# Performance work log

Measured on AMD Instinct MI355X. Metric: run time of the kernel, lower is better.

The kernel has to match this reference:

```python
import jax, jax.numpy as jnp
import numpy as np

C = 64
CR = C // 8  # reduced channels for Q/K


def _conv1x1(x, W, b):
    # 1x1 conv == per-pixel linear over channels: x [b,c,h,w], W [o,c], b [o]
    return jnp.einsum('bchw,oc->bohw', x, W) + b[None, :, None, None]


def setup_inputs() -> dict:
    key = jax.random.key(0)
    ks = jax.random.split(key, 12)
    b, c, h, w = 8, C, 48, 48
    s = 1.0 / np.sqrt(c)
    inp = {
        'x1': jax.random.normal(ks[0], (b, c, h, w), jnp.float32),
        'x2': jax.random.normal(ks[1], (b, c, h, w), jnp.float32),
        'Wqk1': jax.random.normal(ks[2], (2 * CR, c), jnp.float32) * s,
        'bqk1': jnp.zeros((2 * CR,), jnp.float32),
        'Wqk2': jax.random.normal(ks[3], (2 * CR, c), jnp.float32) * s,
        'bqk2': jnp.zeros((2 * CR,), jnp.float32),
        'Wv1': jax.random.normal(ks[4], (c, c), jnp.float32) * s,
        'bv1': jnp.zeros((c,), jnp.float32),
        'Wv2': jax.random.normal(ks[5], (c, c), jnp.float32) * s,
        'bv2': jnp.zeros((c,), jnp.float32),
        'gamma': jnp.zeros((1,), jnp.float32) + 0.1,  # nonzero so output depends on attn
        'beta': jnp.zeros((1,), jnp.float32) + 0.1,
    }
    return inp


def reference(x1, x2, Wqk1, bqk1, Wqk2, bqk2, Wv1, bv1, Wv2, bv2, gamma, beta):
    b, c, h, w = x1.shape
    n = h * w
    qk1 = _conv1x1(x1, Wqk1, bqk1)
    qk2 = _conv1x1(x2, Wqk2, bqk2)
    q1, k1 = qk1[:, :CR], qk1[:, CR:]
    q2, k2 = qk2[:, :CR], qk2[:, CR:]
    # flatten spatial: [b, cr, n]
    q1 = q1.reshape(b, CR, n); k1 = k1.reshape(b, CR, n)
    q2 = q2.reshape(b, CR, n); k2 = k2.reshape(b, CR, n)
    v1 = _conv1x1(x1, Wv1, bv1).reshape(b, c, n)
    v2 = _conv1x1(x2, Wv2, bv2).reshape(b, c, n)
    # attn[b,i,j] = softmax_j( q[:, :, i] . k[:, :, j] )
    attn1 = jax.nn.softmax(jnp.einsum('bci,bcj->bij', q1, k1), axis=-1)
    attn2 = jax.nn.softmax(jnp.einsum('bci,bcj->bij', q2, k2), axis=-1)
    # out[:, :, j] = sum_i v[:, :, i] * attn[:, i, j]
    o1 = jnp.einsum('bci,bij->bcj', v1, attn2).reshape(b, c, h, w) * gamma + x1
    o2 = jnp.einsum('bci,bij->bcj', v2, attn1).reshape(b, c, h, w) * beta + x2
    return (o1, o2)
```

## Files before the change

kernel.cpp:

```cpp
#include <hip/hip_runtime.h>
#include <hip/hip_bf16.h>

#define NB   8
#define CCH  64
#define CR8  8
#define NPX  2304
#define BCN  (NB*CCH*NPX)
#define LOG2E 1.4426950408889634f

typedef short  short8   __attribute__((ext_vector_type(8)));
typedef unsigned short ushort8t __attribute__((ext_vector_type(8)));
typedef float  float4t  __attribute__((ext_vector_type(4)));
typedef float  float16t __attribute__((ext_vector_type(16)));

static __device__ __forceinline__ float fexp2(float x) {
    return __builtin_amdgcn_exp2f(x);
}
static __device__ __forceinline__ unsigned short bf16r(float f) {
    return (unsigned short)((__float_as_uint(f) + 0x8000u) >> 16);
}
static __device__ __forceinline__ unsigned int pack_bf16(float lo, float hi) {
    const unsigned int ul = __float_as_uint(lo) + 0x8000u;
    const unsigned int uh = __float_as_uint(hi) + 0x8000u;
    return __builtin_amdgcn_perm(uh, ul, 0x07060302u);
}
static __device__ __forceinline__ short8 pack8(const float* f) {
    union { unsigned int u[4]; short8 s; } r;
    #pragma unroll
    for (int j = 0; j < 4; j++) r.u[j] = pack_bf16(f[2*j], f[2*j+1]);
    return r.s;
}

static __device__ __forceinline__ void build_bfrag(const float16t sc, short8* bf) {
    unsigned int d[4][2];
    #pragma unroll
    for (int q = 0; q < 4; q++) {
        #pragma unroll
        for (int m = 0; m < 2; m++)
            d[q][m] = pack_bf16(fexp2(sc[4*q + 2*m]), fexp2(sc[4*q + 2*m + 1]));
    }
    #pragma unroll
    for (int kp = 0; kp < 2; kp++) {
        union { unsigned int u[4]; short8 s; } r;
        #pragma unroll
        for (int m = 0; m < 2; m++) {
            unsigned int x = d[2*kp][m];
            unsigned int y = d[2*kp + 1][m];
            asm("v_permlane32_swap_b32 %0, %1" : "+v"(x), "+v"(y));
            r.u[m]     = x;
            r.u[2 + m] = y;
        }
        bf[kp] = r.s;
    }
}

#define WS_QB1 0
#define WS_KB1 (WS_QB1 + 147456)
#define WS_QB2 (WS_KB1 + 147456)
#define WS_KB2 (WS_QB2 + 147456)
#define WS_V1  (WS_KB2 + 147456)
#define WS_V2  (WS_V1 + BCN/2)

__global__ __launch_bounds__(256) void proj_kernel(
    const float* __restrict__ x1, const float* __restrict__ x2,
    const float* __restrict__ Wqk1, const float* __restrict__ bqk1,
    const float* __restrict__ Wqk2, const float* __restrict__ bqk2,
    const float* __restrict__ Wv1,  const float* __restrict__ bv1,
    const float* __restrict__ Wv2,  const float* __restrict__ bv2,
    float* __restrict__ ws, float* __restrict__ out)
{
    const int t    = threadIdx.x;
    const int lane = t & 63;
    const int w    = t >> 6;
    const int n16  = lane & 15;
    const int c4   = lane >> 4;
    const int nt   = w & 1;
    const int mh   = w >> 1;
    const int b    = blockIdx.y;
    const int px   = blockIdx.x * 32 + nt * 16 + n16;

    const float* xsb[2];
    xsb[0] = x1 + ((size_t)b * CCH) * NPX + px;
    xsb[1] = x2 + ((size_t)b * CCH) * NPX + px;

    float xr[2][16];
    short8 bfrag[2][2];
    #pragma unroll
    for (int st = 0; st < 2; st++) {
        #pragma unroll
        for (int ch = 0; ch < 2; ch++) {
            #pragma unroll
            for (int j = 0; j < 8; j++)
                xr[st][ch * 8 + j] = xsb[st][(ch * 32 + c4 * 8 + j) * NPX];
            bfrag[st][ch] = pack8(&xr[st][ch * 8]);
        }
    }

    if (mh == 0) {
        #pragma unroll
        for (int st = 0; st < 2; st++) {
            float* outs = out + (st ? (size_t)BCN : 0);
            #pragma unroll
            for (int e = 0; e < 16; e++) {
                const int ch = (e >> 3) * 32 + c4 * 8 + (e & 7);
                outs[((size_t)b * CCH + ch) * NPX + px] = xr[st][e];
            }
        }
    }

    float4t acc[5];
    #pragma unroll
    for (int mt = 0; mt < 5; mt++) { acc[mt][0]=0.f; acc[mt][1]=0.f; acc[mt][2]=0.f; acc[mt][3]=0.f; }

    #pragma unroll
    for (int mt = 0; mt < 5; mt++) {
        const int mi  = mh * 5 + mt;
        const int isqk = (mi < 2);
        const int st  = isqk ? (mi & 1) : (mi >= 6);
        const float* Wb;
        int rowbase;
        if (isqk) { Wb = (mi == 0) ? Wqk1 : Wqk2; rowbase = 0; }
        else      { Wb = (mi >= 6) ? Wv2 : Wv1; rowbase = (mi - (mi >= 6 ? 6 : 2)) * 16; }
        const float* wrow = Wb + (size_t)(rowbase + n16) * 64 + c4 * 8;

        const short8 bf0 = st ? bfrag[1][0] : bfrag[0][0];
        const short8 bf1 = st ? bfrag[1][1] : bfrag[0][1];

        #pragma unroll
        for (int ch = 0; ch < 2; ch++) {
            float fa[8];
            const float4 a0 = *(const float4*)(wrow + ch * 32);
            const float4 a1 = *(const float4*)(wrow + ch * 32 + 4);
            fa[0] = a0.x; fa[1] = a0.y; fa[2] = a0.z; fa[3] = a0.w;
            fa[4] = a1.x; fa[5] = a1.y; fa[6] = a1.z; fa[7] = a1.w;
            acc[mt] = __builtin_amdgcn_mfma_f32_16x16x32_bf16(
                pack8(fa), ch ? bf1 : bf0, acc[mt], 0, 0, 0);
        }
    }

    #pragma unroll
    for (int mt = 0; mt < 5; mt++) {
        const int mi = mh * 5 + mt;
        if (mi < 2) {
            const int st = mi & 1;
            const float* bqk = st ? bqk2 : bqk1;
            unsigned short* qb = (unsigned short*)(ws + (st ? WS_QB2 : WS_QB1));
            unsigned short* kb = (unsigned short*)(ws + (st ? WS_KB2 : WS_KB1));
            const size_t rbase = (size_t)(b * NPX + px) * 16;
            #pragma unroll
            for (int r = 0; r < 4; r++) {
                const int oc = c4 * 4 + r;
                const float val = acc[mt][r] + bqk[oc];
                if (oc < 8)
                    qb[rbase + oc] = bf16r(val * LOG2E);
                else
                    kb[rbase + (oc - 8)] = bf16r(val);
            }
            ushort8t zq, zk;
            #pragma unroll
            for (int e = 0; e < 8; e++) { zq[e] = 0; zk[e] = 0; }
            zk[0] = 0x3F80; zk[1] = 0x3F80;
            if (c4 == 0) *(ushort8t*)(qb + rbase + 8) = zq;
            if (c4 == 2) *(ushort8t*)(kb + rbase + 8) = zk;
        } else {
            const int st = (mi >= 6);
            const int vt_ = mi - (st ? 6 : 2);
            const float* bv = st ? bv2 : bv1;
            unsigned short* v = (unsigned short*)(ws + (st ? WS_V2 : WS_V1));
            #pragma unroll
            for (int r = 0; r < 4; r++) {
                const int oc = vt_ * 16 + c4 * 4 + r;
                const float val = acc[mt][r] + bv[oc];
                v[((size_t)b * CCH + oc) * NPX + px] = bf16r(val);
            }
        }
    }
}

__global__ __launch_bounds__(256) void stats_kernel(float* __restrict__ ws)
{
    const int t  = threadIdx.x;
    const int w  = t >> 6;
    const int n  = t & 31;
    const int h  = (t & 63) >> 5;
    const int ig = blockIdx.x;
    const int ab = blockIdx.y;
    const int b  = ab & 7;
    const int a  = ab >> 3;

    unsigned short* qbw = (unsigned short*)(ws + (a ? WS_QB2 : WS_QB1));
    const unsigned short* qb = qbw;
    const unsigned short* kb = (const unsigned short*)(ws + (a ? WS_KB2 : WS_KB1));

    __shared__ float red[4][32];

    const short8 qf = *(const short8*)(qb + (size_t)(b * NPX + ig * 32 + n) * 16 + h * 8);

    const unsigned short* kp = kb + (size_t)(b * NPX + w * 576 + n) * 16 + h * 8;
    short8 kf = *(const short8*)kp;

    float ssum = 0.f;
    for (int jc = 0; jc < 18; jc++) {
        kp += 512;
        short8 kn = kf;
        if (jc + 1 < 18) kn = *(const short8*)kp;
        float16t acc = {};
        acc = __builtin_amdgcn_mfma_f32_32x32x16_bf16(kf, qf, acc, 0, 0, 0);
        float s0 = 0.f, s1 = 0.f, s2 = 0.f, s3 = 0.f;
        #pragma unroll
        for (int r = 0; r < 4; r++) {
            s0 += fexp2(acc[4 * r + 0]);
            s1 += fexp2(acc[4 * r + 1]);
            s2 += fexp2(acc[4 * r + 2]);
            s3 += fexp2(acc[4 * r + 3]);
        }
        ssum += (s0 + s1) + (s2 + s3);
        kf = kn;
    }
    ssum += __shfl_xor(ssum, 32);
    if (h == 0) red[w][n] = ssum;
    __syncthreads();

    if (t < 32) {
        const float d = (red[0][t] + red[1][t]) + (red[2][t] + red[3][t]);
        const float m = -__log2f(d);
        const unsigned short mhi = bf16r(m);
        __hip_bfloat16 hb; *(unsigned short*)&hb = mhi;
        const unsigned short mlo = bf16r(m - __bfloat162float(hb));
        const size_t rbase = (size_t)(b * NPX + ig * 32 + t) * 16;
        qbw[rbase + 8] = mhi;
        qbw[rbase + 9] = mlo;
    }
}

__global__ __launch_bounds__(256) void out_kernel(
    const float* __restrict__ gamma, const float* __restrict__ beta,
    const float* __restrict__ ws, float* __restrict__ out)
{
    const int t  = threadIdx.x;
    const int jt = blockIdx.x;
    const int b  = blockIdx.y;
    const int z  = blockIdx.z;
    const int o  = z >> 1;
    const int g  = z & 1;

    const int a = o ? 0 : 1;
    const unsigned short* qb = (const unsigned short*)(ws + (a ? WS_QB2 : WS_QB1));
    const unsigned short* kb = (const unsigned short*)(ws + (a ? WS_KB2 : WS_KB1));
    const unsigned short* v  = (const unsigned short*)(ws + (o ? WS_V2 : WS_V1));
    const float  scale = o ? beta[0] : gamma[0];

    __shared__ unsigned short vt[2][64][72];

    const int lane = t & 63;
    const int w    = t >> 6;
    const int n    = lane & 31;
    const int h    = lane >> 5;
    const int jh   = w & 1;
    const int ih   = w >> 1;

    const int j0 = jt * 64 + jh * 32;

    const short8 kfrag = *(const short8*)(kb + (size_t)(b * NPX + j0 + n) * 16 + h * 8);

    const int c0 = t >> 3, s80 = (t & 7) * 8;
    const int c1 = (t + 256) >> 3, s81 = ((t + 256) & 7) * 8;

    const int ibase = g * 1152;
    const unsigned short* vp0 = v + ((size_t)b * CCH + c0) * NPX + ibase + s80;
    const unsigned short* vp1 = v + ((size_t)b * CCH + c1) * NPX + ibase + s81;
    const unsigned short* qp  = qb + (size_t)(b * NPX + ibase + ih * 32 + n) * 16 + h * 8;

    {
        const float4 va = *(const float4*)vp0;
        const float4 vb = *(const float4*)vp1;
        *(float4*)&vt[0][c0][s80] = va;
        *(float4*)&vt[0][c1][s81] = vb;
    }
    short8 qf = *(const short8*)qp;

    float16t oacc0 = {}, oacc1 = {};
    int cur = 0;

    for (int it = 0; it < 18; it++) {
        vp0 += 64; vp1 += 64; qp += 64 * 16;
        float4 vn0, vn1;
        short8 qn = qf;
        if (it + 1 < 18) {
            vn0 = *(const float4*)vp0;
            vn1 = *(const float4*)vp1;
            qn  = *(const short8*)qp;
        }

        __syncthreads();

        float16t sc = {};
        sc = __builtin_amdgcn_mfma_f32_32x32x16_bf16(qf, kfrag, sc, 0, 0, 0);

        short8 bf[2];
        build_bfrag(sc, bf);

        {
            const short8 a0 = *(const short8*)&vt[cur][n][ih * 32 + 0 * 16 + h * 8];
            const short8 a1 = *(const short8*)&vt[cur][32 + n][ih * 32 + 0 * 16 + h * 8];
            oacc0 = __builtin_amdgcn_mfma_f32_32x32x16_bf16(a0, bf[0], oacc0, 0, 0, 0);
            oacc1 = __builtin_amdgcn_mfma_f32_32x32x16_bf16(a1, bf[0], oacc1, 0, 0, 0);
            const short8 a2 = *(const short8*)&vt[cur][n][ih * 32 + 1 * 16 + h * 8];
            const short8 a3 = *(const short8*)&vt[cur][32 + n][ih * 32 + 1 * 16 + h * 8];
            oacc0 = __builtin_amdgcn_mfma_f32_32x32x16_bf16(a2, bf[1], oacc0, 0, 0, 0);
            oacc1 = __builtin_amdgcn_mfma_f32_32x32x16_bf16(a3, bf[1], oacc1, 0, 0, 0);
        }

        if (it + 1 < 18) {
            *(float4*)&vt[cur ^ 1][c0][s80] = vn0;
            *(float4*)&vt[cur ^ 1][c1][s81] = vn1;
        }

        qf = qn;
        cur ^= 1;
    }

    __syncthreads();
    float* comb = (float*)&vt[0][0][0];
    float* cb = comb + (size_t)jh * 2304 + (size_t)lane * 36;
    if (ih == 1) {
        *(float4*)(cb +  0) = *((const float4*)&oacc0 + 0);
        *(float4*)(cb +  4) = *((const float4*)&oacc0 + 1);
        *(float4*)(cb +  8) = *((const float4*)&oacc0 + 2);
        *(float4*)(cb + 12) = *((const float4*)&oacc0 + 3);
        *(float4*)(cb + 16) = *((const float4*)&oacc1 + 0);
        *(float4*)(cb + 20) = *((const float4*)&oacc1 + 1);
        *(float4*)(cb + 24) = *((const float4*)&oacc1 + 2);
        *(float4*)(cb + 28) = *((const float4*)&oacc1 + 3);
    }
    __syncthreads();
    if (ih == 0) {
        #pragma unroll
        for (int q = 0; q < 4; q++) {
            const float4 p0 = *(const float4*)(cb + q * 4);
            const float4 p1 = *(const float4*)(cb + 16 + q * 4);
            oacc0[4*q+0] += p0.x; oacc0[4*q+1] += p0.y; oacc0[4*q+2] += p0.z; oacc0[4*q+3] += p0.w;
            oacc1[4*q+0] += p1.x; oacc1[4*q+1] += p1.y; oacc1[4*q+2] += p1.z; oacc1[4*q+3] += p1.w;
        }
        float* outp = out + (o ? BCN : 0) + (b * CCH) * NPX + j0 + n;
        #pragma unroll
        for (int r = 0; r < 16; r++) {
            const int row = (r & 3) + 8 * (r >> 2) + 4 * h;
            atomicAdd(outp + row * NPX, oacc0[r] * scale);
            atomicAdd(outp + (32 + row) * NPX, oacc1[r] * scale);
        }
    }
}

extern "C" void kernel_launch(void* const* d_in, const int* in_sizes, int n_in,
                              void* d_out, int out_size, void* d_ws, size_t ws_size,
                              hipStream_t stream)
{
    const float* x1   = (const float*)d_in[0];
    const float* x2   = (const float*)d_in[1];
    const float* Wqk1 = (const float*)d_in[2];
    const float* bqk1 = (const float*)d_in[3];
    const float* Wqk2 = (const float*)d_in[4];
    const float* bqk2 = (const float*)d_in[5];
    const float* Wv1  = (const float*)d_in[6];
    const float* bv1  = (const float*)d_in[7];
    const float* Wv2  = (const float*)d_in[8];
    const float* bv2  = (const float*)d_in[9];
    const float* gamma = (const float*)d_in[10];
    const float* beta  = (const float*)d_in[11];
    float* out = (float*)d_out;
    float* ws  = (float*)d_ws;

    proj_kernel<<<dim3(72, 8), 256, 0, stream>>>(
        x1, x2, Wqk1, bqk1, Wqk2, bqk2, Wv1, bv1, Wv2, bv2, ws, out);
    stats_kernel<<<dim3(72, 16), 256, 0, stream>>>(ws);
    out_kernel<<<dim3(36, 8, 4), 256, 0, stream>>>(gamma, beta, ws, out);
}
```

Measured before the change: 138.3 us.

## Split output kernel across channel halves instead of key-range halves, drop atomics

```diff
diff --git a/kernel.cpp b/kernel.cpp
--- a/kernel.cpp
+++ b/kernel.cpp
@@ -250,7 +250,7 @@
     const unsigned short* v  = (const unsigned short*)(ws + (o ? WS_V2 : WS_V1));
     const float  scale = o ? beta[0] : gamma[0];
 
-    __shared__ unsigned short vt[2][64][72];
+    __shared__ unsigned short vt[2][32][72];
 
     const int lane = t & 63;
     const int w    = t >> 6;
@@ -259,36 +259,28 @@
     const int jh   = w & 1;
     const int ih   = w >> 1;
 
-    const int j0 = jt * 64 + jh * 32;
+    const int j0    = jt * 64 + jh * 32;
+    const int cbase = g * 32;
 
     const short8 kfrag = *(const short8*)(kb + (size_t)(b * NPX + j0 + n) * 16 + h * 8);
 
     const int c0 = t >> 3, s80 = (t & 7) * 8;
-    const int c1 = (t + 256) >> 3, s81 = ((t + 256) & 7) * 8;
-
-    const int ibase = g * 1152;
-    const unsigned short* vp0 = v + ((size_t)b * CCH + c0) * NPX + ibase + s80;
-    const unsigned short* vp1 = v + ((size_t)b * CCH + c1) * NPX + ibase + s81;
-    const unsigned short* qp  = qb + (size_t)(b * NPX + ibase + ih * 32 + n) * 16 + h * 8;
-
-    {
-        const float4 va = *(const float4*)vp0;
-        const float4 vb = *(const float4*)vp1;
-        *(float4*)&vt[0][c0][s80] = va;
-        *(float4*)&vt[0][c1][s81] = vb;
-    }
+
+    const unsigned short* vp0 = v + ((size_t)b * CCH + cbase + c0) * NPX + s80;
+    const unsigned short* qp  = qb + (size_t)(b * NPX + ih * 32 + n) * 16 + h * 8;
+
+    *(float4*)&vt[0][c0][s80] = *(const float4*)vp0;
     short8 qf = *(const short8*)qp;
 
-    float16t oacc0 = {}, oacc1 = {};
+    float16t oacc = {};
     int cur = 0;
 
-    for (int it = 0; it < 18; it++) {
-        vp0 += 64; vp1 += 64; qp += 64 * 16;
-        float4 vn0, vn1;
+    for (int it = 0; it < 36; it++) {
+        vp0 += 64; qp += 64 * 16;
+        float4 vn0;
         short8 qn = qf;
-        if (it + 1 < 18) {
+        if (it + 1 < 36) {
             vn0 = *(const float4*)vp0;
-            vn1 = *(const float4*)vp1;
             qn  = *(const short8*)qp;
         }
 
@@ -302,19 +294,13 @@
 
         {
             const short8 a0 = *(const short8*)&vt[cur][n][ih * 32 + 0 * 16 + h * 8];
-            const short8 a1 = *(const short8*)&vt[cur][32 + n][ih * 32 + 0 * 16 + h * 8];
-            oacc0 = __builtin_amdgcn_mfma_f32_32x32x16_bf16(a0, bf[0], oacc0, 0, 0, 0);
-            oacc1 = __builtin_amdgcn_mfma_f32_32x32x16_bf16(a1, bf[0], oacc1, 0, 0, 0);
+            oacc = __builtin_amdgcn_mfma_f32_32x32x16_bf16(a0, bf[0], oacc, 0, 0, 0);
             const short8 a2 = *(const short8*)&vt[cur][n][ih * 32 + 1 * 16 + h * 8];
-            const short8 a3 = *(const short8*)&vt[cur][32 + n][ih * 32 + 1 * 16 + h * 8];
-            oacc0 = __builtin_amdgcn_mfma_f32_32x32x16_bf16(a2, bf[1], oacc0, 0, 0, 0);
-            oacc1 = __builtin_amdgcn_mfma_f32_32x32x16_bf16(a3, bf[1], oacc1, 0, 0, 0);
-        }
-
-        if (it + 1 < 18) {
+            oacc = __builtin_amdgcn_mfma_f32_32x32x16_bf16(a2, bf[1], oacc, 0, 0, 0);
+        }
+
+        if (it + 1 < 36)
             *(float4*)&vt[cur ^ 1][c0][s80] = vn0;
-            *(float4*)&vt[cur ^ 1][c1][s81] = vn1;
-        }
 
         qf = qn;
         cur ^= 1;
@@ -322,32 +308,26 @@
 
     __syncthreads();
     float* comb = (float*)&vt[0][0][0];
-    float* cb = comb + (size_t)jh * 2304 + (size_t)lane * 36;
+    float* cb = comb + (size_t)jh * 1024 + (size_t)lane * 16;
     if (ih == 1) {
-        *(float4*)(cb +  0) = *((const float4*)&oacc0 + 0);
-        *(float4*)(cb +  4) = *((const float4*)&oacc0 + 1);
-        *(float4*)(cb +  8) = *((const float4*)&oacc0 + 2);
-        *(float4*)(cb + 12) = *((const float4*)&oacc0 + 3);
-        *(float4*)(cb + 16) = *((const float4*)&oacc1 + 0);
-        *(float4*)(cb + 20) = *((const float4*)&oacc1 + 1);
-        *(float4*)(cb + 24) = *((const float4*)&oacc1 + 2);
-        *(float4*)(cb + 28) = *((const float4*)&oacc1 + 3);
+        *(float4*)(cb +  0) = *((const float4*)&oacc + 0);
+        *(float4*)(cb +  4) = *((const float4*)&oacc + 1);
+        *(float4*)(cb +  8) = *((const float4*)&oacc + 2);
+        *(float4*)(cb + 12) = *((const float4*)&oacc + 3);
     }
     __syncthreads();
     if (ih == 0) {
         #pragma unroll
         for (int q = 0; q < 4; q++) {
             const float4 p0 = *(const float4*)(cb + q * 4);
-            const float4 p1 = *(const float4*)(cb + 16 + q * 4);
-            oacc0[4*q+0] += p0.x; oacc0[4*q+1] += p0.y; oacc0[4*q+2] += p0.z; oacc0[4*q+3] += p0.w;
-            oacc1[4*q+0] += p1.x; oacc1[4*q+1] += p1.y; oacc1[4*q+2] += p1.z; oacc1[4*q+3] += p1.w;
-        }
-        float* outp = out + (o ? BCN : 0) + (b * CCH) * NPX + j0 + n;
+            oacc[4*q+0] += p0.x; oacc[4*q+1] += p0.y; oacc[4*q+2] += p0.z; oacc[4*q+3] += p0.w;
+        }
+        float* outp = out + (o ? BCN : 0) + (b * CCH + cbase) * NPX + j0 + n;
         #pragma unroll
         for (int r = 0; r < 16; r++) {
             const int row = (r & 3) + 8 * (r >> 2) + 4 * h;
-            atomicAdd(outp + row * NPX, oacc0[r] * scale);
-            atomicAdd(outp + (32 + row) * NPX, oacc1[r] * scale);
+            float* p = outp + row * NPX;
+            *p += oacc[r] * scale;
         }
     }
 }
```

After: 142.2 us. 2.8% more time.
